# Kernel tuning notes

Hardware: AMD Instinct MI355X
Metric: run time of the kernel (lower is better)

## Reference

```python
import jax, jax.numpy as jnp
import numpy as np
from itertools import permutations, combinations

BATCH = 32768
EPS = 1e-06  # positivity eps from __init__


def _levi_civita7():
    e = np.zeros((7,) * 7, dtype=np.float32)
    for p in permutations(range(7)):
        inv = sum(1 for i in range(7) for j in range(i + 1, 7) if p[i] > p[j])
        e[p] = -1.0 if inv % 2 else 1.0
    return jnp.asarray(e)

_EPS7 = _levi_civita7()  # (7,7,7,7,7,7,7) rank-7 Levi-Civita tensor
_TRIPLES = np.array(list(combinations(range(7), 3)), dtype=np.int32)  # (35,3) i<j<k index triples
_PERMS3 = [((0, 1, 2), 1.0), ((1, 2, 0), 1.0), ((2, 0, 1), 1.0),
           ((0, 2, 1), -1.0), ((2, 1, 0), -1.0), ((1, 0, 2), -1.0)]


def _phi_full(phi):
    # expand 35 independent components to fully antisymmetric (B,7,7,7)
    b = phi.shape[0]
    pf = jnp.zeros((b, 7, 7, 7), phi.dtype)
    for perm, s in _PERMS3:
        ia = _TRIPLES[:, perm[0]]
        ib = _TRIPLES[:, perm[1]]
        ic = _TRIPLES[:, perm[2]]
        pf = pf.at[:, ia, ib, ic].set(s * phi)
    return pf


def _metric_from_phi(phi):
    # Standard G2 metric: B_ij = (1/144) phi_ikl phi_jmn phi_pqr eps^{klmnpqr};
    # g = B / |det B|^{1/9}  (unit-determinant normalization)
    pf = _phi_full(phi)  # (B,7,7,7)
    C = jnp.einsum('klmnpqr,bpqr->bklmn', _EPS7, pf)  # (B,7,7,7,7)
    T = jnp.einsum('bklmn,bjmn->bklj', C, pf)          # (B,7,7,7)
    Bm = jnp.einsum('bikl,bklj->bij', pf, T) / 144.0   # (B,7,7)
    det = jnp.linalg.det(Bm)
    g = Bm / (jnp.abs(det)[:, None, None] + 1e-12) ** (1.0 / 9.0)
    return 0.5 * (g + jnp.swapaxes(g, -1, -2))  # exact symmetry for eigvalsh


def setup_inputs() -> dict:
    key = jax.random.key(0)
    phi = jax.random.normal(key, (BATCH, 35), dtype=jnp.float32)
    return {"phi": phi}


def reference(phi):
    g = _metric_from_phi(phi)              # (B,7,7)
    ev = jnp.linalg.eigvalsh(g)            # (B,7)
    return jax.nn.relu(-ev + EPS).sum(axis=-1)  # (B,) sum of negative-eigenvalue violations
```

## Files before the change

kernel.cpp:

```cpp
#include <hip/hip_runtime.h>
#include <utility>

#define BATCH 32768
#define NPHI 35
#define SWEEPS 6

constexpr int choose2(int n){ return (n*(n-1))/2; }

constexpr int tri_id_sorted(int a,int b,int c){
  int id=0;
  for(int x=0;x<a;++x) id += choose2(6-x);
  for(int y=a+1;y<b;++y) id += (6-y);
  id += (c-b-1);
  return id;
}

constexpr int tri_id3(int a,int b,int c){
  int x=a,y=b,z=c;
  if (x>y){int t=x;x=y;y=t;}
  if (y>z){int t=y;y=z;z=t;}
  if (x>y){int t=x;x=y;y=t;}
  return tri_id_sorted(x,y,z);
}

constexpr int sgn3(int a,int b,int c){
  int inv = (a>b)+(a>c)+(b>c);
  return (inv&1)? -1 : 1;
}

constexpr int UT(int i,int j){
  return i*7 - (i*(i-1))/2 + (j-i);
}

constexpr int pair_k(int g){
  int idx=0;
  for(int k=0;k<7;++k) for(int l=k+1;l<7;++l){ if(idx==g) return k; ++idx; }
  return 0;
}
constexpr int pair_l(int g){
  int idx=0;
  for(int k=0;k<7;++k) for(int l=k+1;l<7;++l){ if(idx==g) return l; ++idx; }
  return 0;
}

struct GProg {
  int nt, nb;
  signed char t_dst[50], t_a[50], t_b[50], t_s[50]; unsigned char t_init[50];
  signed char b_dst[26], b_a[26], b_b[26], b_s[26];
};

constexpr GProg build_group(int k,int l){
  GProg P{}; P.nt=0; P.nb=0;
  bool tinit[7]={};
  for(int m=0;m<7;++m) for(int n2=m+1;n2<7;++n2){
    if(m==k||m==l||n2==k||n2==l) continue;
    int comp[3]={0,0,0}; int cn=0;
    for(int x=0;x<7;++x) if(x!=k&&x!=l&&x!=m&&x!=n2){ comp[cn]=x; ++cn; }
    int perm[7]={k,l,m,n2,comp[0],comp[1],comp[2]};
    int invc=0;
    for(int i=0;i<7;++i) for(int j=i+1;j<7;++j) if(perm[i]>perm[j]) ++invc;
    const int es=(invc&1)? -1 : 1;
    const int tcomp=tri_id_sorted(comp[0],comp[1],comp[2]);
    for(int j=0;j<7;++j){
      if(j==m||j==n2) continue;
      P.t_dst[P.nt]=(signed char)j;
      P.t_a [P.nt]=(signed char)tcomp;
      P.t_b [P.nt]=(signed char)tri_id3(j,m,n2);
      P.t_s [P.nt]=(signed char)(es*sgn3(j,m,n2));
      P.t_init[P.nt]=tinit[j]?0:1; tinit[j]=true;
      ++P.nt;
    }
  }
  for(int i=0;i<7;++i){
    if(i==k||i==l) continue;
    for(int j=i;j<7;++j){
      P.b_dst[P.nb]=(signed char)UT(i,j);
      P.b_a [P.nb]=(signed char)tri_id3(i,k,l);
      P.b_b [P.nb]=(signed char)j;
      P.b_s [P.nb]=(signed char)sgn3(i,k,l);
      ++P.nb;
    }
  }
  return P;
}

template<int G> inline constexpr GProg GP = build_group(pair_k(G), pair_l(G));

template<int G,int Q>
__device__ __forceinline__ void t_step(float (&T)[7], const float (&ph)[NPHI]){
  constexpr int d=GP<G>.t_dst[Q], a=GP<G>.t_a[Q], b=GP<G>.t_b[Q];
  constexpr bool neg=(GP<G>.t_s[Q]<0), ini=(GP<G>.t_init[Q]!=0);
  const float x = neg ? -ph[a] : ph[a];
  if constexpr (ini) T[d] = x*ph[b];
  else               T[d] = fmaf(x, ph[b], T[d]);
}

template<int G,int Q>
__device__ __forceinline__ void b_step(float (&U)[28], const float (&T)[7],
                                       const float (&ph)[NPHI]){
  constexpr int d=GP<G>.b_dst[Q], a=GP<G>.b_a[Q], b=GP<G>.b_b[Q];
  constexpr bool neg=(GP<G>.b_s[Q]<0);
  const float x = neg ? -ph[a] : ph[a];
  U[d] = fmaf(x, T[b], U[d]);
}

template<int G,int... TQ>
__device__ __forceinline__ void run_t(float (&T)[7], const float (&ph)[NPHI],
                                      std::integer_sequence<int,TQ...>){
  (t_step<G,TQ>(T,ph), ...);
}
template<int G,int... BQ>
__device__ __forceinline__ void run_b(float (&U)[28], const float (&T)[7],
                                      const float (&ph)[NPHI],
                                      std::integer_sequence<int,BQ...>){
  (b_step<G,BQ>(U,T,ph), ...);
}

template<int G>
__device__ __forceinline__ void do_group(float (&U)[28], const float (&ph)[NPHI]){
  float T[7];
  run_t<G>(T, ph, std::make_integer_sequence<int, GP<G>.nt>{});
  run_b<G>(U, T, ph, std::make_integer_sequence<int, GP<G>.nb>{});
  __builtin_amdgcn_sched_barrier(0);
}

template<int... G>
__device__ __forceinline__ void all_groups(float (&U)[28], const float (&ph)[NPHI],
                                           std::integer_sequence<int,G...>){
  (do_group<G>(U,ph), ...);
}

__global__ __launch_bounds__(64,1)
void PositivityConstraint_89086211654295_kernel(const float* __restrict__ phi,
                                                float* __restrict__ out){
  const int gid = blockIdx.x*64 + threadIdx.x;

  const float* __restrict__ p = phi + (size_t)gid * NPHI;
  float ph[NPHI];
  #pragma unroll
  for (int i=0;i<NPHI;++i) ph[i] = p[i];

  float U[28];
  #pragma unroll
  for (int i=0;i<28;++i) U[i]=0.f;

  all_groups(U, ph, std::make_integer_sequence<int,21>{});

  float A[28];
  #pragma unroll
  for (int i=0;i<28;++i) A[i] = U[i]*(1.0f/6.0f);

  for (int sweep=0; sweep<SWEEPS; ++sweep){
    #pragma unroll
    for (int p1=0;p1<7;++p1){
      #pragma unroll
      for (int q1=p1+1;q1<7;++q1){
        const float apq = A[UT(p1,q1)];
        const float app = A[UT(p1,p1)];
        const float aqq = A[UT(q1,q1)];
        const float s2  = apq + apq;
        const float h   = aqq - app;
        const float w   = fmaf(s2, s2, h*h);
        const float r   = __builtin_amdgcn_sqrtf(w);
        const float den = fabsf(h) + r + 1e-38f;
        const float rc  = __builtin_amdgcn_rcpf(den);
        float t = s2 * rc;
        t = (h < 0.0f) ? -t : t;
        const float c = __builtin_amdgcn_rsqf(fmaf(t,t,1.0f));
        const float s = t*c;
        A[UT(p1,p1)] = fmaf(-t, apq, app);
        A[UT(q1,q1)] = fmaf( t, apq, aqq);
        A[UT(p1,q1)] = 0.0f;
        #pragma unroll
        for (int r2=0;r2<7;++r2){
          if (r2==p1 || r2==q1) continue;
          const int irp = (r2<p1)? UT(r2,p1) : UT(p1,r2);
          const int irq = (r2<q1)? UT(r2,q1) : UT(q1,r2);
          const float arp = A[irp], arq = A[irq];
          A[irp] = fmaf(c, arp, -(s*arq));
          A[irq] = fmaf(c, arq,  (s*arp));
        }
      }
    }
  }

  float det = 1.0f;
  #pragma unroll
  for (int i=0;i<7;++i) det *= A[UT(i,i)];
  const float ad = fabsf(det) + 1e-12f;
  const float scale = __builtin_amdgcn_exp2f(__builtin_amdgcn_logf(ad) * (1.0f/9.0f));
  const float inv = __builtin_amdgcn_rcpf(scale);

  float sum = 0.0f;
  #pragma unroll
  for (int i=0;i<7;++i){
    const float ev = A[UT(i,i)]*inv;
    sum += fmaxf(1e-6f - ev, 0.0f);
  }
  out[gid] = sum;
}

extern "C" void kernel_launch(void* const* d_in, const int* in_sizes, int n_in,
                              void* d_out, int out_size, void* d_ws, size_t ws_size,
                              hipStream_t stream) {
  const float* phi = (const float*)d_in[0];
  float* out = (float*)d_out;
  (void)in_sizes; (void)n_in; (void)out_size; (void)d_ws; (void)ws_size;
  hipLaunchKernelGGL(PositivityConstraint_89086211654295_kernel,
                     dim3(BATCH/64), dim3(64), 0, stream, phi, out);
}
```

Baseline: 65.83 us.

## Process two batch elements per thread with interleaved Jacobi rotations

Each thread now loads and processes two phi vectors (e and e+B/2), interleaving metric construction and Jacobi rotations for instruction-level parallelism, and the grid is halved. The rotation's sign handling is also simplified with copysign. This aims to hide ALU/transcendental latency in the dependent Jacobi chain, at the cost of doubled register usage and half as many waves across the GPU.

After: 90.44 us. 37.4% more time.

```diff
diff --git a/kernel.cpp b/kernel.cpp
--- a/kernel.cpp
+++ b/kernel.cpp
@@ -117,87 +117,104 @@
 }
 
 template<int G>
-__device__ __forceinline__ void do_group(float (&U)[28], const float (&ph)[NPHI]){
-  float T[7];
-  run_t<G>(T, ph, std::make_integer_sequence<int, GP<G>.nt>{});
-  run_b<G>(U, T, ph, std::make_integer_sequence<int, GP<G>.nb>{});
+__device__ __forceinline__ void do_group2(float (&U0)[28], float (&U1)[28],
+                                          const float (&p0)[NPHI],
+                                          const float (&p1)[NPHI]){
+  float T0[7], T1[7];
+  run_t<G>(T0, p0, std::make_integer_sequence<int, GP<G>.nt>{});
+  run_t<G>(T1, p1, std::make_integer_sequence<int, GP<G>.nt>{});
+  run_b<G>(U0, T0, p0, std::make_integer_sequence<int, GP<G>.nb>{});
+  run_b<G>(U1, T1, p1, std::make_integer_sequence<int, GP<G>.nb>{});
   __builtin_amdgcn_sched_barrier(0);
 }
 
 template<int... G>
-__device__ __forceinline__ void all_groups(float (&U)[28], const float (&ph)[NPHI],
-                                           std::integer_sequence<int,G...>){
-  (do_group<G>(U,ph), ...);
+__device__ __forceinline__ void all_groups2(float (&U0)[28], float (&U1)[28],
+                                            const float (&p0)[NPHI],
+                                            const float (&p1)[NPHI],
+                                            std::integer_sequence<int,G...>){
+  (do_group2<G>(U0,U1,p0,p1), ...);
+}
+
+__device__ __forceinline__ void jrot(float (&A)[28], int p1, int q1){
+  const float apq = A[UT(p1,q1)];
+  const float app = A[UT(p1,p1)];
+  const float aqq = A[UT(q1,q1)];
+  const float s2  = apq + apq;
+  const float h   = aqq - app;
+  const float r   = __builtin_amdgcn_sqrtf(fmaf(s2, s2, h*h));
+  const float den = h + __builtin_copysignf(r + 1e-38f, h);
+  const float t   = s2 * __builtin_amdgcn_rcpf(den);
+  const float c   = __builtin_amdgcn_rsqf(fmaf(t, t, 1.0f));
+  const float s   = t*c;
+  A[UT(p1,p1)] = fmaf(-t, apq, app);
+  A[UT(q1,q1)] = fmaf( t, apq, aqq);
+  A[UT(p1,q1)] = 0.0f;
+  #pragma unroll
+  for (int r2=0;r2<7;++r2){
+    if (r2==p1 || r2==q1) continue;
+    const int irp = (r2<p1)? UT(r2,p1) : UT(p1,r2);
+    const int irq = (r2<q1)? UT(r2,q1) : UT(q1,r2);
+    const float arp = A[irp], arq = A[irq];
+    A[irp] = fmaf(c, arp, -(s*arq));
+    A[irq] = fmaf(c, arq,  (s*arp));
+  }
+}
+
+__device__ __forceinline__ float finish(const float (&A)[28]){
+  float det = 1.0f;
+  #pragma unroll
+  for (int i=0;i<7;++i) det *= A[UT(i,i)];
+  const float ad = fabsf(det) + 1e-12f;
+  const float scale = __builtin_amdgcn_exp2f(__builtin_amdgcn_logf(ad) * (1.0f/9.0f));
+  const float inv = __builtin_amdgcn_rcpf(scale);
+  float sum = 0.0f;
+  #pragma unroll
+  for (int i=0;i<7;++i){
+    const float ev = A[UT(i,i)]*inv;
+    sum += fmaxf(1e-6f - ev, 0.0f);
+  }
+  return sum;
 }
 
 __global__ __launch_bounds__(64,1)
 void PositivityConstraint_89086211654295_kernel(const float* __restrict__ phi,
                                                 float* __restrict__ out){
   const int gid = blockIdx.x*64 + threadIdx.x;
-
-  const float* __restrict__ p = phi + (size_t)gid * NPHI;
-  float ph[NPHI];
-  #pragma unroll
-  for (int i=0;i<NPHI;++i) ph[i] = p[i];
-
-  float U[28];
-  #pragma unroll
-  for (int i=0;i<28;++i) U[i]=0.f;
-
-  all_groups(U, ph, std::make_integer_sequence<int,21>{});
-
-  float A[28];
-  #pragma unroll
-  for (int i=0;i<28;++i) A[i] = U[i]*(1.0f/6.0f);
+  const int e0 = gid;
+  const int e1 = gid + BATCH/2;
+
+  const float* __restrict__ pA = phi + (size_t)e0 * NPHI;
+  const float* __restrict__ pB = phi + (size_t)e1 * NPHI;
+  float ph0[NPHI], ph1[NPHI];
+  #pragma unroll
+  for (int i=0;i<NPHI;++i) ph0[i] = pA[i];
+  #pragma unroll
+  for (int i=0;i<NPHI;++i) ph1[i] = pB[i];
+
+  float U0[28], U1[28];
+  #pragma unroll
+  for (int i=0;i<28;++i){ U0[i]=0.f; U1[i]=0.f; }
+
+  all_groups2(U0, U1, ph0, ph1, std::make_integer_sequence<int,21>{});
+
+  float A0[28], A1[28];
+  #pragma unroll
+  for (int i=0;i<28;++i){ A0[i]=U0[i]*(1.0f/6.0f); A1[i]=U1[i]*(1.0f/6.0f); }
 
   for (int sweep=0; sweep<SWEEPS; ++sweep){
     #pragma unroll
     for (int p1=0;p1<7;++p1){
       #pragma unroll
       for (int q1=p1+1;q1<7;++q1){
-        const float apq = A[UT(p1,q1)];
-        const float app = A[UT(p1,p1)];
-        const float aqq = A[UT(q1,q1)];
-        const float s2  = apq + apq;
-        const float h   = aqq - app;
-        const float w   = fmaf(s2, s2, h*h);
-        const float r   = __builtin_amdgcn_sqrtf(w);
-        const float den = fabsf(h) + r + 1e-38f;
-        const float rc  = __builtin_amdgcn_rcpf(den);
-        float t = s2 * rc;
-        t = (h < 0.0f) ? -t : t;
-        const float c = __builtin_amdgcn_rsqf(fmaf(t,t,1.0f));
-        const float s = t*c;
-        A[UT(p1,p1)] = fmaf(-t, apq, app);
-        A[UT(q1,q1)] = fmaf( t, apq, aqq);
-        A[UT(p1,q1)] = 0.0f;
-        #pragma unroll
-        for (int r2=0;r2<7;++r2){
-          if (r2==p1 || r2==q1) continue;
-          const int irp = (r2<p1)? UT(r2,p1) : UT(p1,r2);
-          const int irq = (r2<q1)? UT(r2,q1) : UT(q1,r2);
-          const float arp = A[irp], arq = A[irq];
-          A[irp] = fmaf(c, arp, -(s*arq));
-          A[irq] = fmaf(c, arq,  (s*arp));
-        }
+        jrot(A0, p1, q1);
+        jrot(A1, p1, q1);
       }
     }
   }
 
-  float det = 1.0f;
-  #pragma unroll
-  for (int i=0;i<7;++i) det *= A[UT(i,i)];
-  const float ad = fabsf(det) + 1e-12f;
-  const float scale = __builtin_amdgcn_exp2f(__builtin_amdgcn_logf(ad) * (1.0f/9.0f));
-  const float inv = __builtin_amdgcn_rcpf(scale);
-
-  float sum = 0.0f;
-  #pragma unroll
-  for (int i=0;i<7;++i){
-    const float ev = A[UT(i,i)]*inv;
-    sum += fmaxf(1e-6f - ev, 0.0f);
-  }
-  out[gid] = sum;
+  out[e0] = finish(A0);
+  out[e1] = finish(A1);
 }
 
 extern "C" void kernel_launch(void* const* d_in, const int* in_sizes, int n_in,
@@ -207,5 +224,5 @@
   float* out = (float*)d_out;
   (void)in_sizes; (void)n_in; (void)out_size; (void)d_ws; (void)ws_size;
   hipLaunchKernelGGL(PositivityConstraint_89086211654295_kernel,
-                     dim3(BATCH/64), dim3(64), 0, stream, phi, out);
-}
+                     dim3(BATCH/2/64), dim3(64), 0, stream, phi, out);
+}
```
